# Performance work log

Measured on AMD Instinct MI355X. Metric: run time of the kernel, lower is better.

## Reference

```python
import jax, jax.numpy as jnp
import numpy as np

EPS = 1e-8
SEARCH = 21  # search_window_size


def _window_stack(x, S):
    """x: [B,C,Hp,Wp] (already padded). Returns [B,C,H,W,S*S] matching
    torch unfold(2,S,1).unfold(3,S,1).reshape(...,-1) ordering (h-offset major)."""
    B, C, Hp, Wp = x.shape
    H, W = Hp - S + 1, Wp - S + 1
    patches = jax.lax.conv_general_dilated_patches(
        x, filter_shape=(S, S), window_strides=(1, 1), padding='VALID',
        dimension_numbers=('NCHW', 'OIHW', 'NCHW'))  # [B, C*S*S, H, W], (C, u, v) major->minor
    patches = patches.reshape(B, C, S * S, H, W)
    return jnp.transpose(patches, (0, 1, 3, 4, 2))  # [B,C,H,W,S*S]


def setup_inputs() -> dict:
    key = jax.random.key(0)
    k1, k2 = jax.random.split(key)
    rgb = jax.random.uniform(k1, (1, 3, 256, 256), dtype=jnp.float32)  # must be in [0,1]
    h = jnp.array([0.1], dtype=jnp.float32)  # learned NLM bandwidth parameter
    return {"rgb": rgb, "h": h}


def reference(rgb, h):
    S = SEARCH
    pad = (S - 1) // 2
    # luminance (clip only affects y, not the rgb values being averaged)
    rgb_c = jnp.clip(rgb, 0.0, 1.0)
    y = 0.299 * rgb_c[:, :1] + 0.587 * rgb_c[:, 1:2] + 0.114 * rgb_c[:, 2:]  # [B,1,H,W]

    pw = ((0, 0), (0, 0), (pad, pad), (pad, pad))
    rgb_ws = _window_stack(jnp.pad(rgb, pw, mode='reflect'), S)  # [B,3,H,W,S^2]
    y_ws = _window_stack(jnp.pad(y, pw, mode='reflect'), S)      # [B,1,H,W,S^2]

    dis = (y[..., None] - y_ws) ** 2                              # [B,1,H,W,S^2]
    dis_pad = jnp.pad(dis, ((0, 0), (0, 0), (pad, pad), (pad, pad), (0, 0)), mode='reflect')
    # sum of squared diffs over an SxS spatial window per offset (matches unfold+sum)
    dis = jax.lax.reduce_window(dis_pad, 0.0, jax.lax.add,
                                (1, 1, S, S, 1), (1, 1, 1, 1, 1), 'VALID')  # [B,1,H,W,S^2]

    distances = jnp.sqrt(jax.nn.relu(dis))
    weights = jnp.exp(-distances / (jax.nn.relu(h) + EPS))        # [B,1,H,W,S^2]
    denoised = (weights * rgb_ws).sum(-1) / weights.sum(-1)       # [B,3,H,W]
    return jnp.clip(denoised, 0.0, 1.0)
```

## Files before the change

### kernel.cpp

```cpp
#include <hip/hip_runtime.h>
#include <math.h>


#define IMG 256
#define NPIX (IMG * IMG)
#define TILE 32
#define GR 52
#define YD 72
#define YSTR 74
#define HST 52
#define NOFF 441
#define NGB 8
#define NTHR 1024
#define NW 16

typedef __attribute__((ext_vector_type(4))) _Float16 half4;
typedef __attribute__((ext_vector_type(2))) _Float16 half2_t;

#if __has_builtin(__builtin_amdgcn_fdot2)
#define FDOT2(a, b, c) __builtin_amdgcn_fdot2((a), (b), (c), false)
#else
#define FDOT2(a, b, c) ((c) + (float)(a).x * (float)(b).x + (float)(a).y * (float)(b).y)
#endif

#if __has_builtin(__builtin_amdgcn_sqrtf)
#define ASQRT(x) __builtin_amdgcn_sqrtf(x)
#else
#define ASQRT(x) sqrtf(x)
#endif

__device__ __forceinline__ int refl(int t) {
    t = t < 0 ? -t : t;
    return t > 255 ? 510 - t : t;
}

template <bool DIRECT>
__global__ __launch_bounds__(NTHR, 4)
void nlm_main(const float* __restrict__ rgb, const float* __restrict__ hptr,
              float4* __restrict__ partials)
{
    __shared__ __align__(16) _Float16 hsT[NW][TILE][HST];
    __shared__ __align__(16) _Float16 Yreg[YD][YSTR];
    __shared__ __align__(16) half2_t  CregRG[GR][GR];
    __shared__ __align__(16) _Float16 CregB[GR][54];
    __shared__ unsigned char cjTab[21][GR];

    const int tid = threadIdx.x;
    const int tj = ((int)blockIdx.x & 7) * TILE;
    const int ti = ((int)blockIdx.x >> 3) * TILE;

    const int Ybi = min(max(ti - 20, 0), IMG - YD);
    const int Ybj = min(max(tj - 20, 0), IMG - YD);
    const bool interior = (ti >= 20) && (ti + 51 <= 255) && (tj >= 20) && (tj + 51 <= 255);

    for (int idx = tid; idx < YD * YD; idx += NTHR) {
        int a = idx / YD, b = idx - a * YD;
        int g = (Ybi + a) * IMG + (Ybj + b);
        float r  = fminf(fmaxf(rgb[g], 0.f), 1.f);
        float gg = fminf(fmaxf(rgb[NPIX + g], 0.f), 1.f);
        float bb = fminf(fmaxf(rgb[2 * NPIX + g], 0.f), 1.f);
        Yreg[a][b] = (_Float16)(0.299f * r + 0.587f * gg + 0.114f * bb);
    }
    for (int idx = tid; idx < GR * GR; idx += NTHR) {
        int t = idx / GR, b = idx - t * GR;
        int g = refl(ti - 10 + t) * IMG + refl(tj - 10 + b);
        half2_t c;
        c.x = (_Float16)rgb[g];
        c.y = (_Float16)rgb[NPIX + g];
        CregRG[t][b] = c;
        CregB[t][b] = (_Float16)rgb[2 * NPIX + g];
    }
    if (!interior) {
        for (int idx = tid; idx < 21 * GR; idx += NTHR) {
            int d = idx / GR, c = idx - d * GR;
            cjTab[d][c] = (unsigned char)(refl(refl(tj - 10 + c) + (d - 10)) - Ybj);
        }
    }
    __syncthreads();

    const int lane = tid & 63;
    const int wv   = tid >> 6;
    const bool hact = lane < GR;

    half2_t y0h[26];
    if (hact) {
        if (interior) {
            const half2_t* q0 = (const half2_t*)&Yreg[lane + 10][10];
            #pragma unroll
            for (int i = 0; i < 26; ++i) y0h[i] = q0[i];
        } else {
            const _Float16* Y0row = &Yreg[refl(ti - 10 + lane) - Ybi][0];
            const unsigned char* cj0 = &cjTab[10][0];
            #pragma unroll
            for (int i = 0; i < 26; ++i) {
                half2_t v;
                v.x = Y0row[cj0[2 * i]];
                v.y = Y0row[cj0[2 * i + 1]];
                y0h[i] = v;
            }
        }
    }

    const float hv = fmaxf(hptr[0], 0.f);
    const float negI = -1.0f / (hv + 1e-8f);

    const int pb  = lane & 31;
    const int s16 = (lane >> 5) << 4;

    half2_t accRG[16], accBW[16];
    #pragma unroll
    for (int k = 0; k < 16; ++k) {
        accRG[k].x = (_Float16)0.f; accRG[k].y = (_Float16)0.f;
        accBW[k].x = (_Float16)0.f; accBW[k].y = (_Float16)0.f;
    }

    half2_t one; one.x = (_Float16)1.f; one.y = (_Float16)1.f;

    const int o0 = (int)blockIdx.y * NW + wv;
    int du = o0 / 21 - 10;
    int dv = o0 % 21 - 10;
    for (int o = o0; o < NOFF; o += NGB * NW) {
        if (hact) {
            const int t = lane;
            half2_t ff[26];
            if (interior) {
                if ((dv & 1) == 0) {
                    const half2_t* q1 = (const half2_t*)&Yreg[t + 10 + du][10 + dv];
                    #pragma unroll
                    for (int i = 0; i < 26; ++i) {
                        half2_t d2 = y0h[i] - q1[i];
                        ff[i] = d2 * d2;
                    }
                } else {
                    const half2_t* q1 = (const half2_t*)&Yreg[t + 10 + du][10 + dv - 1];
                    half2_t prev = q1[0];
                    #pragma unroll
                    for (int i = 0; i < 26; ++i) {
                        half2_t cur = q1[i + 1];
                        half2_t b; b.x = prev.y; b.y = cur.x;
                        half2_t d2 = y0h[i] - b;
                        ff[i] = d2 * d2;
                        prev = cur;
                    }
                }
            } else {
                const unsigned int* cw = (const unsigned int*)&cjTab[dv + 10][0];
                const _Float16* Y1row = &Yreg[refl(refl(ti - 10 + t) + du) - Ybi][0];
                #pragma unroll
                for (int i = 0; i < 26; ++i) {
                    unsigned int w0 = cw[i >> 1];
                    int sh = (i & 1) * 16;
                    _Float16 a0 = Y1row[(w0 >> sh) & 0xffu];
                    _Float16 a1 = Y1row[(w0 >> (sh + 8)) & 0xffu];
                    half2_t yv; yv.x = a0; yv.y = a1;
                    half2_t d2 = y0h[i] - yv;
                    ff[i] = d2 * d2;
                }
            }
            float s0f = 0.f, s1f = 0.f;
            #pragma unroll
            for (int i = 0; i < 10; ++i) s0f = FDOT2(ff[i], one, s0f);
            s0f += (float)ff[10].x;
            #pragma unroll
            for (int i = 8; i < 18; ++i) s1f = FDOT2(ff[i], one, s1f);
            s1f += (float)ff[18].x;
            _Float16 sA = (_Float16)s0f;
            _Float16 sB = (_Float16)s1f;
            hsT[wv][0][t]  = sA;
            hsT[wv][16][t] = sB;
            #pragma unroll
            for (int k = 1; k < 16; ++k) {
                {
                    int ja = 20 + k, jb = k - 1;
                    _Float16 fa = (ja & 1) ? ff[ja >> 1].y : ff[ja >> 1].x;
                    _Float16 fb = (jb & 1) ? ff[jb >> 1].y : ff[jb >> 1].x;
                    sA += (_Float16)(fa - fb);
                    hsT[wv][k][t] = sA;
                }
                {
                    int ja = 36 + k, jb = 15 + k;
                    _Float16 fa = (ja & 1) ? ff[ja >> 1].y : ff[ja >> 1].x;
                    _Float16 fb = (jb & 1) ? ff[jb >> 1].y : ff[jb >> 1].x;
                    sB += (_Float16)(fa - fb);
                    hsT[wv][16 + k][t] = sB;
                }
            }
        }

        {
            const half2_t* col2 = (const half2_t*)&hsT[wv][pb][s16];
            half2_t w2[18];
            #pragma unroll
            for (int i = 0; i < 18; ++i) w2[i] = col2[i];

            float vs0 = 0.f, vs1 = 0.f;
            #pragma unroll
            for (int i = 0; i < 10; ++i) vs0 = FDOT2(w2[i], one, vs0);
            vs0 += (float)w2[10].x;
            #pragma unroll
            for (int i = 4; i < 14; ++i) vs1 = FDOT2(w2[i], one, vs1);
            vs1 += (float)w2[14].x;

            float vss[16];
            vss[0] = vs0;
            vss[8] = vs1;
            #pragma unroll
            for (int k = 0; k < 7; ++k) {
                {
                    int ja = 21 + k, jb = k;
                    _Float16 fa = (ja & 1) ? w2[ja >> 1].y : w2[ja >> 1].x;
                    _Float16 fb = (jb & 1) ? w2[jb >> 1].y : w2[jb >> 1].x;
                    vss[k + 1] = vss[k] + (float)(_Float16)(fa - fb);
                }
                {
                    int ja = 29 + k, jb = 8 + k;
                    _Float16 fa = (ja & 1) ? w2[ja >> 1].y : w2[ja >> 1].x;
                    _Float16 fb = (jb & 1) ? w2[jb >> 1].y : w2[jb >> 1].x;
                    vss[k + 9] = vss[k + 8] + (float)(_Float16)(fa - fb);
                }
            }

            const int cr = s16 + 10 + du;
            const int cc = pb + 10 + dv;
            #pragma unroll
            for (int k = 0; k < 16; ++k) {
                float dist = ASQRT(fmaxf(vss[k], 0.f));
                float w = __expf(dist * negI);
                _Float16 wh = (_Float16)w;
                half2_t w2v; w2v.x = wh; w2v.y = wh;
                half2_t cRG = CregRG[cr + k][cc];
                union { unsigned int u; half2_t h; } cv;
                cv.u = (unsigned int)(*(const unsigned short*)&CregB[cr + k][cc]) | 0x3C000000u;
                half2_t cBW = cv.h;
                accRG[k] = w2v * cRG + accRG[k];
                accBW[k] = w2v * cBW + accBW[k];
            }
        }

        du += 6; dv += 2;
        if (dv > 10) { dv -= 21; du += 1; }
    }

    __syncthreads();
    float4* scratch = (float4*)&hsT[0][0][0];
    #pragma unroll
    for (int w = 0; w < NW; ++w) {
        if (wv == w) {
            #pragma unroll
            for (int k = 0; k < 16; ++k) {
                int px = (s16 + k) * 32 + pb;
                float4 v = make_float4((float)accRG[k].x, (float)accRG[k].y,
                                       (float)accBW[k].x, (float)accBW[k].y);
                if (w == 0) scratch[px] = v;
                else {
                    float4 a = scratch[px];
                    scratch[px] = make_float4(a.x + v.x, a.y + v.y, a.z + v.z, a.w + v.w);
                }
            }
        }
        __syncthreads();
    }
    for (int i = tid; i < TILE * TILE; i += NTHR) {
        float4 v = scratch[i];
        int gpix = (ti + (i >> 5)) * IMG + (tj + (i & 31));
        if (DIRECT) {
            partials[(size_t)blockIdx.y * NPIX + gpix] = v;
        } else {
            float* p = (float*)&partials[gpix];
            atomicAdd(p + 0, v.x);
            atomicAdd(p + 1, v.y);
            atomicAdd(p + 2, v.z);
            atomicAdd(p + 3, v.w);
        }
    }
}

template <int NGT>
__global__ __launch_bounds__(256)
void nlm_finalize(const float4* __restrict__ partials, float* __restrict__ out)
{
    int idx = blockIdx.x * blockDim.x + threadIdx.x;
    float r = 0.f, g = 0.f, b = 0.f, w = 0.f;
    #pragma unroll
    for (int gg = 0; gg < NGT; ++gg) {
        float4 p = partials[(size_t)gg * NPIX + idx];
        r += p.x; g += p.y; b += p.z; w += p.w;
    }
    float inv = 1.0f / w;
    out[idx]            = fminf(fmaxf(r * inv, 0.f), 1.f);
    out[NPIX + idx]     = fminf(fmaxf(g * inv, 0.f), 1.f);
    out[2 * NPIX + idx] = fminf(fmaxf(b * inv, 0.f), 1.f);
}

extern "C" void kernel_launch(void* const* d_in, const int* in_sizes, int n_in,
                              void* d_out, int out_size, void* d_ws, size_t ws_size,
                              hipStream_t stream) {
    (void)in_sizes; (void)n_in; (void)out_size;
    const float* rgb  = (const float*)d_in[0];
    const float* hptr = (const float*)d_in[1];
    float* out = (float*)d_out;
    float4* partials = (float4*)d_ws;

    const bool direct = ws_size >= (size_t)NGB * NPIX * sizeof(float4);
    dim3 grid(64, NGB);
    if (direct) {
        nlm_main<true><<<grid, NTHR, 0, stream>>>(rgb, hptr, partials);
        nlm_finalize<NGB><<<NPIX / 256, 256, 0, stream>>>(partials, out);
    } else {
        (void)hipMemsetAsync(partials, 0, (size_t)NPIX * sizeof(float4), stream);
        nlm_main<false><<<grid, NTHR, 0, stream>>>(rgb, hptr, partials);
        nlm_finalize<1><<<NPIX / 256, 256, 0, stream>>>(partials, out);
    }
}
```

Baseline: 111.6 us.

## Use smaller blocks with more offset groups and compute reflection indices on the fly

Halves the block to 512 threads (8 waves) and spreads the 441 offsets over 12 block groups instead of 8, with the group count as a template parameter, so more, smaller blocks fill the GPU and the launch-bounds occupancy hint rises from 4 to 6. The per-offset column reflection table is replaced by a single 52-entry column map. Reflection is recomputed arithmetically only for tiles at the left or right edge; other border tiles use a plain offset. In exchange it writes and reduces 12 partial planes in the finalize pass instead of 8, which adds global memory traffic, and the on-the-fly index math adds ALU work on edge tiles.

```diff
diff --git a/kernel.cpp b/kernel.cpp
--- a/kernel.cpp
+++ b/kernel.cpp
@@ -10,9 +10,8 @@
 #define YSTR 74
 #define HST 52
 #define NOFF 441
-#define NGB 8
-#define NTHR 1024
-#define NW 16
+#define NTHR 512
+#define NW 8
 
 typedef __attribute__((ext_vector_type(4))) _Float16 half4;
 typedef __attribute__((ext_vector_type(2))) _Float16 half2_t;
@@ -34,16 +33,16 @@
     return t > 255 ? 510 - t : t;
 }
 
-template <bool DIRECT>
-__global__ __launch_bounds__(NTHR, 4)
+template <bool DIRECT, int GROUPS>
+__global__ __launch_bounds__(NTHR, 6)
 void nlm_main(const float* __restrict__ rgb, const float* __restrict__ hptr,
               float4* __restrict__ partials)
 {
     __shared__ __align__(16) _Float16 hsT[NW][TILE][HST];
     __shared__ __align__(16) _Float16 Yreg[YD][YSTR];
     __shared__ __align__(16) half2_t  CregRG[GR][GR];
-    __shared__ __align__(16) _Float16 CregB[GR][54];
-    __shared__ unsigned char cjTab[21][GR];
+    __shared__ __align__(16) _Float16 CregB[GR][GR];
+    __shared__ __align__(16) unsigned char mTab[64];
 
     const int tid = threadIdx.x;
     const int tj = ((int)blockIdx.x & 7) * TILE;
@@ -52,6 +51,7 @@
     const int Ybi = min(max(ti - 20, 0), IMG - YD);
     const int Ybj = min(max(tj - 20, 0), IMG - YD);
     const bool interior = (ti >= 20) && (ti + 51 <= 255) && (tj >= 20) && (tj + 51 <= 255);
+    const bool colRefl = (tj == 0) || (tj == IMG - TILE);
 
     for (int idx = tid; idx < YD * YD; idx += NTHR) {
         int a = idx / YD, b = idx - a * YD;
@@ -70,12 +70,7 @@
         CregRG[t][b] = c;
         CregB[t][b] = (_Float16)rgb[2 * NPIX + g];
     }
-    if (!interior) {
-        for (int idx = tid; idx < 21 * GR; idx += NTHR) {
-            int d = idx / GR, c = idx - d * GR;
-            cjTab[d][c] = (unsigned char)(refl(refl(tj - 10 + c) + (d - 10)) - Ybj);
-        }
-    }
+    if (tid < GR) mTab[tid] = (unsigned char)refl(tj - 10 + tid);
     __syncthreads();
 
     const int lane = tid & 63;
@@ -90,12 +85,11 @@
             for (int i = 0; i < 26; ++i) y0h[i] = q0[i];
         } else {
             const _Float16* Y0row = &Yreg[refl(ti - 10 + lane) - Ybi][0];
-            const unsigned char* cj0 = &cjTab[10][0];
             #pragma unroll
             for (int i = 0; i < 26; ++i) {
                 half2_t v;
-                v.x = Y0row[cj0[2 * i]];
-                v.y = Y0row[cj0[2 * i + 1]];
+                v.x = Y0row[(int)mTab[2 * i]     - Ybj];
+                v.y = Y0row[(int)mTab[2 * i + 1] - Ybj];
                 y0h[i] = v;
             }
         }
@@ -116,10 +110,13 @@
 
     half2_t one; one.x = (_Float16)1.f; one.y = (_Float16)1.f;
 
+    constexpr int STEP = GROUPS * NW;
+    constexpr int DDU = STEP / 21;
+    constexpr int DDV = STEP % 21;
     const int o0 = (int)blockIdx.y * NW + wv;
     int du = o0 / 21 - 10;
     int dv = o0 % 21 - 10;
-    for (int o = o0; o < NOFF; o += NGB * NW) {
+    for (int o = o0; o < NOFF; o += STEP) {
         if (hact) {
             const int t = lane;
             half2_t ff[26];
@@ -144,17 +141,37 @@
                     }
                 }
             } else {
-                const unsigned int* cw = (const unsigned int*)&cjTab[dv + 10][0];
+                const unsigned int* mw = (const unsigned int*)mTab;
                 const _Float16* Y1row = &Yreg[refl(refl(ti - 10 + t) + du) - Ybi][0];
-                #pragma unroll
-                for (int i = 0; i < 26; ++i) {
-                    unsigned int w0 = cw[i >> 1];
-                    int sh = (i & 1) * 16;
-                    _Float16 a0 = Y1row[(w0 >> sh) & 0xffu];
-                    _Float16 a1 = Y1row[(w0 >> (sh + 8)) & 0xffu];
-                    half2_t yv; yv.x = a0; yv.y = a1;
-                    half2_t d2 = y0h[i] - yv;
-                    ff[i] = d2 * d2;
+                if (colRefl) {
+                    #pragma unroll
+                    for (int i = 0; i < 26; ++i) {
+                        unsigned int w0 = mw[i >> 1];
+                        int sh = (i & 1) * 16;
+                        int g0 = (int)((w0 >> sh) & 0xffu) + dv;
+                        g0 = g0 < 0 ? -g0 : g0;
+                        g0 = min(g0, 510 - g0);
+                        int g1 = (int)((w0 >> (sh + 8)) & 0xffu) + dv;
+                        g1 = g1 < 0 ? -g1 : g1;
+                        g1 = min(g1, 510 - g1);
+                        half2_t yv;
+                        yv.x = Y1row[g0 - Ybj];
+                        yv.y = Y1row[g1 - Ybj];
+                        half2_t d2 = y0h[i] - yv;
+                        ff[i] = d2 * d2;
+                    }
+                } else {
+                    const int koff = dv - Ybj;
+                    #pragma unroll
+                    for (int i = 0; i < 26; ++i) {
+                        unsigned int w0 = mw[i >> 1];
+                        int sh = (i & 1) * 16;
+                        _Float16 a0 = Y1row[(int)((w0 >> sh) & 0xffu) + koff];
+                        _Float16 a1 = Y1row[(int)((w0 >> (sh + 8)) & 0xffu) + koff];
+                        half2_t yv; yv.x = a0; yv.y = a1;
+                        half2_t d2 = y0h[i] - yv;
+                        ff[i] = d2 * d2;
+                    }
                 }
             }
             float s0f = 0.f, s1f = 0.f;
@@ -237,7 +254,7 @@
             }
         }
 
-        du += 6; dv += 2;
+        du += DDU; dv += DDV;
         if (dv > 10) { dv -= 21; du += 1; }
     }
 
@@ -301,14 +318,16 @@
     float* out = (float*)d_out;
     float4* partials = (float4*)d_ws;
 
-    const bool direct = ws_size >= (size_t)NGB * NPIX * sizeof(float4);
-    dim3 grid(64, NGB);
-    if (direct) {
-        nlm_main<true><<<grid, NTHR, 0, stream>>>(rgb, hptr, partials);
-        nlm_finalize<NGB><<<NPIX / 256, 256, 0, stream>>>(partials, out);
+    const size_t plane = (size_t)NPIX * sizeof(float4);
+    if (ws_size >= 12 * plane) {
+        nlm_main<true, 12><<<dim3(64, 12), NTHR, 0, stream>>>(rgb, hptr, partials);
+        nlm_finalize<12><<<NPIX / 256, 256, 0, stream>>>(partials, out);
+    } else if (ws_size >= 8 * plane) {
+        nlm_main<true, 8><<<dim3(64, 8), NTHR, 0, stream>>>(rgb, hptr, partials);
+        nlm_finalize<8><<<NPIX / 256, 256, 0, stream>>>(partials, out);
     } else {
-        (void)hipMemsetAsync(partials, 0, (size_t)NPIX * sizeof(float4), stream);
-        nlm_main<false><<<grid, NTHR, 0, stream>>>(rgb, hptr, partials);
+        (void)hipMemsetAsync(partials, 0, plane, stream);
+        nlm_main<false, 12><<<dim3(64, 12), NTHR, 0, stream>>>(rgb, hptr, partials);
         nlm_finalize<1><<<NPIX / 256, 256, 0, stream>>>(partials, out);
     }
 }
```

Result: slower. 116.9 us (+4.7%).
